# Performance work log

Hardware: AMD Instinct MI355X
Metric: run time of the kernel (lower is better)

The kernel has to match this reference:

```python
import jax, jax.numpy as jnp
import numpy as np

VOCAB, F, H1, H2 = 64, 4096, 64, 32   # vocab size, featureVectorSize, hidden dims (hard-coded 64/32/1 in source)
NBBOX, NWORDS = 8192, 16


def _uniform(key, shape, fan_in):
    # torch nn.Linear default init: U(-1/sqrt(fan_in), 1/sqrt(fan_in))
    bound = 1.0 / np.sqrt(fan_in)
    return jax.random.uniform(key, shape, jnp.float32, -bound, bound)


def setup_inputs() -> dict:
    key = jax.random.key(0)
    ks = jax.random.split(key, 8)
    x = jax.random.normal(ks[0], (NBBOX, F), jnp.float32)
    words = jax.random.randint(ks[1], (NWORDS,), 0, VOCAB)  # indices of active word-models
    # Stacked per-word MLP params (one tiny MLP per vocab word)
    W1 = _uniform(ks[2], (VOCAB, F, H1), F)
    b1 = _uniform(ks[3], (VOCAB, H1), F)
    W2 = _uniform(ks[4], (VOCAB, H1, H2), H1)
    b2 = _uniform(ks[5], (VOCAB, H2), H1)
    W3 = _uniform(ks[6], (VOCAB, H2), H2)   # Linear(32,1) weight, squeezed to [VOCAB, H2]
    b3 = _uniform(ks[7], (VOCAB,), H2)
    return {"nBBox": NBBOX, "x": x, "words": words,
            "W1": W1, "b1": b1, "W2": W2, "b2": b2, "W3": W3, "b3": b3}


def reference(nBBox, x, words, W1, b1, W2, b2, W3, b3):
    # Gather the active word-models (dict lookup in the original)
    w1, c1 = W1[words], b1[words]          # [W,F,H1], [W,H1]
    w2, c2 = W2[words], b2[words]          # [W,H1,H2], [W,H2]
    w3, c3 = W3[words], b3[words]          # [W,H2], [W]
    # Batched 3-layer MLP over all active words at once (replaces Python loop)
    h1 = jax.nn.relu(jnp.einsum('bf,wfh->wbh', x, w1) + c1[:, None, :])   # [W,B,H1]
    h2 = jax.nn.relu(jnp.einsum('wbh,whk->wbk', h1, w2) + c2[:, None, :])  # [W,B,H2]
    logits = jnp.einsum('wbk,wk->wb', h2, w3) + c3[:, None]                # [W,B]
    # output = ones(nBBox,1) * prod_w sigmoid(logits_w)
    return jnp.prod(jax.nn.sigmoid(logits), axis=0)[:, None]               # [B,1]
```

## Files before the change

### kernel.cpp

```cpp
#include <hip/hip_runtime.h>
#include <stdint.h>
#include <math.h>

#define NBBOX 8192
#define FDIM  4096
#define H1DIM 64
#define H2DIM 32
#define NW    16

typedef __attribute__((ext_vector_type(8))) _Float16 f16x8;
typedef __attribute__((ext_vector_type(4))) float    f32x4;

typedef __attribute__((address_space(1))) void* gptr_t;
typedef __attribute__((address_space(3))) void* lptr_t;

__device__ __forceinline__ void g2l16(const void* g, void* l) {
    __builtin_amdgcn_global_load_lds((gptr_t)(uintptr_t)g,
                                     (lptr_t)(uint32_t)(uintptr_t)l,
                                     16, 0, 0);
}

__device__ __forceinline__ f16x8 cvt8(float4 a, float4 b) {
    f16x8 h;
    h[0] = (_Float16)a.x; h[1] = (_Float16)a.y; h[2] = (_Float16)a.z; h[3] = (_Float16)a.w;
    h[4] = (_Float16)b.x; h[5] = (_Float16)b.y; h[6] = (_Float16)b.z; h[7] = (_Float16)b.w;
    return h;
}

__global__ __launch_bounds__(256) void prep(
    const float* __restrict__ W1, const int* __restrict__ words,
    uint32_t* __restrict__ bth_u32)
{
    __shared__ uint32_t t[64 * 69];
    const int tid = threadIdx.x;
    const int wi = blockIdx.x >> 5;
    const int ft = blockIdx.x & 31;
    const int f0 = ft * 128;
    const int w  = words[wi];
    const int c    = tid & 63;
    const int fgrp = tid >> 6;

    const float* src = W1 + ((size_t)w * FDIM + f0) * H1DIM + c;
#pragma unroll
    for (int p = 0; p < 16; ++p) {
        const int f = fgrp * 2 + p * 8;
        float v0 = src[(size_t)f * H1DIM];
        float v1 = src[(size_t)(f + 1) * H1DIM];
        union { _Float16 h[2]; uint32_t u; } pk;
        pk.h[0] = (_Float16)v0; pk.h[1] = (_Float16)v1;
        t[c * 69 + (f >> 1)] = pk.u;
    }
    __syncthreads();
#pragma unroll
    for (int p = 0; p < 16; ++p) {
        const int cc = p * 4 + (tid >> 6);
        const int fd = tid & 63;
        bth_u32[(size_t)(wi * 64 + cc) * (FDIM / 2) + ft * 64 + fd] = t[cc * 69 + fd];
    }
}

__global__ __launch_bounds__(256, 2) void gemm_fused(
    const float* __restrict__ x, const _Float16* __restrict__ bth,
    const float* __restrict__ b1, const int* __restrict__ words,
    const float* __restrict__ W2, const float* __restrict__ b2,
    const float* __restrict__ W3, const float* __restrict__ b3,
    float* __restrict__ sig)
{
    __shared__ __align__(16) char smem[65536];
    float* tile = (float*)smem;

    const int mt   = blockIdx.x & 63;
    const int nt   = blockIdx.x >> 6;
    const int t    = threadIdx.x;
    const int w    = t >> 6;
    const int lane = t & 63;
    const int m0 = mt * 128, n0 = nt * 128;

    f32x4 acc[4][4] = {};

    const int lr = lane >> 3;
    const int cg = lane & 7;
    const float*    Ag = x   + (size_t)(m0 + w * 32 + lr) * FDIM + cg * 8;
    const _Float16* Bg = bth + (size_t)(n0 + w * 32 + lr) * FDIM + ((cg ^ lr) * 8);
    const int lwb = w * 4096;

    const int wm = w >> 1, wn = w & 1;
    const int ml = lane & 15;
    const int qw = lane >> 4;

    float4 rA[8], rB[8];

#define STAGE_A_LOAD(R, KT) do { \
    _Pragma("unroll") \
    for (int c = 0; c < 4; ++c) { \
        const float* ap = Ag + (size_t)(c * 8) * FDIM + (size_t)(KT) * 64; \
        R[2 * c]     = *(const float4*)(ap); \
        R[2 * c + 1] = *(const float4*)(ap + 4); \
    } } while (0)

#define STAGE_B(KT, NB) do { \
    _Pragma("unroll") \
    for (int c = 0; c < 4; ++c) \
        g2l16(Bg + (size_t)(c * 8) * FDIM + (size_t)(KT) * 64, \
              smem + (NB) + 16384 + lwb + c * 1024); \
    } while (0)

#define WRITE_A(R, NB) do { \
    _Pragma("unroll") \
    for (int c = 0; c < 4; ++c) \
        *(f16x8*)(smem + (NB) + (w * 32 + c * 8 + lr) * 128 + ((cg ^ lr) * 16)) = \
            cvt8(R[2 * c], R[2 * c + 1]); \
    } while (0)

#define MFMA_PHASE(BUF) do { \
    const _Float16* Ab = (const _Float16*)(smem + (BUF)); \
    const _Float16* Bb = (const _Float16*)(smem + (BUF) + 16384); \
    _Pragma("unroll") \
    for (int s = 0; s < 2; ++s) { \
        f16x8 af[4], bfr[4]; \
        _Pragma("unroll") \
        for (int i = 0; i < 4; ++i) { \
            const int ra = wm * 64 + i * 16 + ml; \
            af[i] = *(const f16x8*)&Ab[ra * 64 + (((s * 4 + qw) ^ (ml & 7)) * 8)]; \
        } \
        _Pragma("unroll") \
        for (int j = 0; j < 4; ++j) { \
            const int rb = wn * 64 + j * 16 + ml; \
            bfr[j] = *(const f16x8*)&Bb[rb * 64 + (((s * 4 + qw) ^ (ml & 7)) * 8)]; \
        } \
        _Pragma("unroll") \
        for (int i = 0; i < 4; ++i) \
            _Pragma("unroll") \
            for (int j = 0; j < 4; ++j) \
                acc[i][j] = __builtin_amdgcn_mfma_f32_16x16x32_f16(af[i], bfr[j], acc[i][j], 0, 0, 0); \
    } } while (0)

    STAGE_A_LOAD(rA, 0);
    STAGE_B(0, 0);
    WRITE_A(rA, 0);
    STAGE_A_LOAD(rB, 1);
    __syncthreads();

    for (int kt = 0; kt < 62; kt += 2) {
        STAGE_A_LOAD(rA, kt + 2);
        STAGE_B(kt + 1, 32768);
        WRITE_A(rB, 32768);
        __builtin_amdgcn_sched_barrier(0);
        MFMA_PHASE(0);
        __syncthreads();
        STAGE_A_LOAD(rB, kt + 3);
        STAGE_B(kt + 2, 0);
        WRITE_A(rA, 0);
        __builtin_amdgcn_sched_barrier(0);
        MFMA_PHASE(32768);
        __syncthreads();
    }
    STAGE_B(63, 32768);
    WRITE_A(rB, 32768);
    __builtin_amdgcn_sched_barrier(0);
    MFMA_PHASE(0);
    __syncthreads();
    MFMA_PHASE(32768);
    __syncthreads();

#undef STAGE_A_LOAD
#undef STAGE_B
#undef WRITE_A
#undef MFMA_PHASE

    const int q  = lane >> 4;
    const int wi = nt * 2 + wn;
    const int wv = __builtin_amdgcn_readfirstlane(words[wi]);
    float* tw = tile + w * 4096;

#pragma unroll
    for (int j = 0; j < 4; ++j) {
        const int col = j * 16 + ml;
        const float bias = b1[wv * H1DIM + col];
        const int c = col >> 2, e = col & 3;
#pragma unroll
        for (int i = 0; i < 4; ++i) {
#pragma unroll
            for (int r = 0; r < 4; ++r) {
                const int row = i * 16 + q * 4 + r;
                const int pos = ((c + row) & 7) | (c & 8);
                float v = acc[i][j][r] + bias;
                tw[row * 64 + pos * 4 + e] = v > 0.f ? v : 0.f;
            }
        }
    }

    const float* W2w = W2 + (size_t)wv * (H1DIM * H2DIM);
    float a2[H2DIM];
#pragma unroll
    for (int j = 0; j < H2DIM; ++j) a2[j] = 0.f;

#pragma unroll
    for (int c2 = 0; c2 < 16; ++c2) {
        const int pos = ((c2 + lane) & 7) | (c2 & 8);
        f32x4 h = *(const f32x4*)&tw[lane * 64 + pos * 4];
#pragma unroll
        for (int kk = 0; kk < 4; ++kk) {
            const float hv = h[kk];
            const int k = c2 * 4 + kk;
#pragma unroll
            for (int j = 0; j < H2DIM; ++j)
                a2[j] = fmaf(hv, W2w[k * H2DIM + j], a2[j]);
        }
    }

    float logit = b3[wv];
#pragma unroll
    for (int j = 0; j < H2DIM; ++j) {
        float h2 = a2[j] + b2[wv * H2DIM + j];
        h2 = h2 > 0.f ? h2 : 0.f;
        logit = fmaf(h2, W3[wv * H2DIM + j], logit);
    }
    sig[(size_t)wi * NBBOX + m0 + wm * 64 + lane] = 1.f / (1.f + expf(-logit));
}

__global__ void prod_k(const float* __restrict__ sig, float* __restrict__ out) {
    const int r = blockIdx.x * 256 + threadIdx.x;
    float p = 1.f;
#pragma unroll
    for (int wi = 0; wi < NW; ++wi) p *= sig[(size_t)wi * NBBOX + r];
    out[r] = p;
}

extern "C" void kernel_launch(void* const* d_in, const int* in_sizes, int n_in,
                              void* d_out, int out_size, void* d_ws, size_t ws_size,
                              hipStream_t stream)
{
    const float* x   = (const float*)d_in[1];
    const int* words = (const int*)  d_in[2];
    const float* W1  = (const float*)d_in[3];
    const float* b1  = (const float*)d_in[4];
    const float* W2  = (const float*)d_in[5];
    const float* b2  = (const float*)d_in[6];
    const float* W3  = (const float*)d_in[7];
    const float* b3  = (const float*)d_in[8];
    float* out = (float*)d_out;

    char* ws = (char*)d_ws;
    _Float16* bth = (_Float16*)(ws);
    float*    sig = (float*)   (ws + 8388608);

    prep<<<512, 256, 0, stream>>>(W1, words, (uint32_t*)bth);
    gemm_fused<<<512, 256, 0, stream>>>(x, bth, b1, words, W2, b2, W3, b3, sig);
    prod_k<<<NBBOX / 256, 256, 0, stream>>>(sig, out);
}
```

Measured before the change: 349.9 us.

## Load fp32 A tiles directly to LDS and convert to fp16 at fragment read

```diff
diff --git a/kernel.cpp b/kernel.cpp
--- a/kernel.cpp
+++ b/kernel.cpp
@@ -18,13 +18,6 @@
     __builtin_amdgcn_global_load_lds((gptr_t)(uintptr_t)g,
                                      (lptr_t)(uint32_t)(uintptr_t)l,
                                      16, 0, 0);
-}
-
-__device__ __forceinline__ f16x8 cvt8(float4 a, float4 b) {
-    f16x8 h;
-    h[0] = (_Float16)a.x; h[1] = (_Float16)a.y; h[2] = (_Float16)a.z; h[3] = (_Float16)a.w;
-    h[4] = (_Float16)b.x; h[5] = (_Float16)b.y; h[6] = (_Float16)b.z; h[7] = (_Float16)b.w;
-    return h;
 }
 
 __global__ __launch_bounds__(256) void prep(
@@ -80,93 +73,81 @@
 
     const int lr = lane >> 3;
     const int cg = lane & 7;
-    const float*    Ag = x   + (size_t)(m0 + w * 32 + lr) * FDIM + cg * 8;
+    const float*    Ag = x   + (size_t)(m0 + w * 32 + lr) * FDIM + ((cg ^ lr) * 4);
     const _Float16* Bg = bth + (size_t)(n0 + w * 32 + lr) * FDIM + ((cg ^ lr) * 8);
     const int lwb = w * 4096;
 
     const int wm = w >> 1, wn = w & 1;
     const int ml = lane & 15;
     const int qw = lane >> 4;
-
-    float4 rA[8], rB[8];
-
-#define STAGE_A_LOAD(R, KT) do { \
-    _Pragma("unroll") \
-    for (int c = 0; c < 4; ++c) { \
-        const float* ap = Ag + (size_t)(c * 8) * FDIM + (size_t)(KT) * 64; \
-        R[2 * c]     = *(const float4*)(ap); \
-        R[2 * c + 1] = *(const float4*)(ap + 4); \
-    } } while (0)
-
-#define STAGE_B(KT, NB) do { \
+    const int x7 = ml & 7;
+
+#define STAGE_A(U, AB) do { \
     _Pragma("unroll") \
     for (int c = 0; c < 4; ++c) \
-        g2l16(Bg + (size_t)(c * 8) * FDIM + (size_t)(KT) * 64, \
-              smem + (NB) + 16384 + lwb + c * 1024); \
+        g2l16(Ag + (size_t)(c * 8) * FDIM + (size_t)(U) * 32, \
+              smem + (AB) + lwb + c * 1024); \
     } while (0)
 
-#define WRITE_A(R, NB) do { \
+#define STAGE_B(V, BB) do { \
     _Pragma("unroll") \
     for (int c = 0; c < 4; ++c) \
-        *(f16x8*)(smem + (NB) + (w * 32 + c * 8 + lr) * 128 + ((cg ^ lr) * 16)) = \
-            cvt8(R[2 * c], R[2 * c + 1]); \
+        g2l16(Bg + (size_t)(c * 8) * FDIM + (size_t)(V) * 64, \
+              smem + (BB) + lwb + c * 1024); \
     } while (0)
 
-#define MFMA_PHASE(BUF) do { \
-    const _Float16* Ab = (const _Float16*)(smem + (BUF)); \
-    const _Float16* Bb = (const _Float16*)(smem + (BUF) + 16384); \
-    _Pragma("unroll") \
-    for (int s = 0; s < 2; ++s) { \
-        f16x8 af[4], bfr[4]; \
+#define STEP(AB, BB, HALF) do { \
+    const char* Abp = smem + (AB); \
+    const char* Bbp = smem + (BB); \
+    f16x8 af[4], bf[4]; \
+    _Pragma("unroll") \
+    for (int i = 0; i < 4; ++i) { \
+        const int ra = wm * 64 + i * 16 + ml; \
+        f32x4 lo = *(const f32x4*)(Abp + ra * 128 + (((2 * qw    ) ^ x7) * 16)); \
+        f32x4 hi = *(const f32x4*)(Abp + ra * 128 + (((2 * qw + 1) ^ x7) * 16)); \
+        f16x8 h; \
+        h[0] = (_Float16)lo[0]; h[1] = (_Float16)lo[1]; \
+        h[2] = (_Float16)lo[2]; h[3] = (_Float16)lo[3]; \
+        h[4] = (_Float16)hi[0]; h[5] = (_Float16)hi[1]; \
+        h[6] = (_Float16)hi[2]; h[7] = (_Float16)hi[3]; \
+        af[i] = h; \
+    } \
+    _Pragma("unroll") \
+    for (int j = 0; j < 4; ++j) { \
+        const int rb = wn * 64 + j * 16 + ml; \
+        bf[j] = *(const f16x8*)(Bbp + rb * 128 + ((((HALF) * 4 + qw) ^ x7) * 16)); \
+    } \
+    _Pragma("unroll") \
+    for (int i = 0; i < 4; ++i) \
         _Pragma("unroll") \
-        for (int i = 0; i < 4; ++i) { \
-            const int ra = wm * 64 + i * 16 + ml; \
-            af[i] = *(const f16x8*)&Ab[ra * 64 + (((s * 4 + qw) ^ (ml & 7)) * 8)]; \
-        } \
-        _Pragma("unroll") \
-        for (int j = 0; j < 4; ++j) { \
-            const int rb = wn * 64 + j * 16 + ml; \
-            bfr[j] = *(const f16x8*)&Bb[rb * 64 + (((s * 4 + qw) ^ (ml & 7)) * 8)]; \
-        } \
-        _Pragma("unroll") \
-        for (int i = 0; i < 4; ++i) \
-            _Pragma("unroll") \
-            for (int j = 0; j < 4; ++j) \
-                acc[i][j] = __builtin_amdgcn_mfma_f32_16x16x32_f16(af[i], bfr[j], acc[i][j], 0, 0, 0); \
-    } } while (0)
-
-    STAGE_A_LOAD(rA, 0);
-    STAGE_B(0, 0);
-    WRITE_A(rA, 0);
-    STAGE_A_LOAD(rB, 1);
-    __syncthreads();
-
-    for (int kt = 0; kt < 62; kt += 2) {
-        STAGE_A_LOAD(rA, kt + 2);
-        STAGE_B(kt + 1, 32768);
-        WRITE_A(rB, 32768);
-        __builtin_amdgcn_sched_barrier(0);
-        MFMA_PHASE(0);
+        for (int j = 0; j < 4; ++j) \
+            acc[i][j] = __builtin_amdgcn_mfma_f32_16x16x32_f16(af[i], bf[j], acc[i][j], 0, 0, 0); \
+    } while (0)
+
+    STAGE_A(0, 0);
+    STAGE_B(0, 32768);
+    __syncthreads();
+
+    for (int v = 0; v < 63; ++v) {
+        const int bb  = 32768 + (v & 1) * 16384;
+        const int bbn = 32768 + ((v + 1) & 1) * 16384;
+        STAGE_A(2 * v + 1, 16384);
+        STAGE_B(v + 1, bbn);
+        STEP(0, bb, 0);
         __syncthreads();
-        STAGE_A_LOAD(rB, kt + 3);
-        STAGE_B(kt + 2, 0);
-        WRITE_A(rA, 0);
-        __builtin_amdgcn_sched_barrier(0);
-        MFMA_PHASE(32768);
+        STAGE_A(2 * v + 2, 0);
+        STEP(16384, bb, 1);
         __syncthreads();
     }
-    STAGE_B(63, 32768);
-    WRITE_A(rB, 32768);
-    __builtin_amdgcn_sched_barrier(0);
-    MFMA_PHASE(0);
-    __syncthreads();
-    MFMA_PHASE(32768);
-    __syncthreads();
-
-#undef STAGE_A_LOAD
+    STAGE_A(127, 16384);
+    STEP(0, 49152, 0);
+    __syncthreads();
+    STEP(16384, 49152, 1);
+    __syncthreads();
+
+#undef STAGE_A
 #undef STAGE_B
-#undef WRITE_A
-#undef MFMA_PHASE
+#undef STEP
 
     const int q  = lane >> 4;
     const int wi = nt * 2 + wn;
```

Measured after the change: 332.4 us. -5.0%, faster.
